# Kernel optimization log

Measured on AMD Instinct MI355X. Metric: run time of the kernel, lower is better.

## Reference

```python
import jax, jax.numpy as jnp
import numpy as np

L = 7
LVL = 3
B = 8
R = 16
N = 4 ** L  # 16384
P = N // 4  # number of local blocks
T = 4 * R   # ConvLocal output features


def build_permutation_indices(L, l):
    delta = 4 ** (L - l - 1)
    tmp = np.tile(np.arange(4) * delta, delta)
    tmp += np.repeat(np.arange(delta), 4)
    tmp = np.tile(tmp, 4 ** l)
    tmp += np.repeat(np.arange(4 ** l) * 4 ** (L - l), 4 ** (L - l))
    return jnp.asarray(tmp, dtype=jnp.int32)


def setup_inputs() -> dict:
    key = jax.random.key(0)
    kx, k1, k2, k3, k4 = jax.random.split(key, 5)
    scale = 1.0 / np.sqrt(T)
    x = jax.random.normal(kx, (B, 2, N, R), dtype=jnp.float32)
    # flax ConvLocal kernels: (out_spatial, kernel_size*in_features, features)
    W_rr = jax.random.normal(k1, (P, 4 * R, T), dtype=jnp.float32) * scale
    W_ri = jax.random.normal(k2, (P, 4 * R, T), dtype=jnp.float32) * scale
    W_ir = jax.random.normal(k3, (P, 4 * R, T), dtype=jnp.float32) * scale
    W_ii = jax.random.normal(k4, (P, 4 * R, T), dtype=jnp.float32) * scale
    perm_idx = build_permutation_indices(L, LVL)
    return {"x": x, "W_rr": W_rr, "W_ri": W_ri, "W_ir": W_ir,
            "W_ii": W_ii, "perm_idx": perm_idx}


def reference(x, W_rr, W_ri, W_ir, W_ii, perm_idx):
    b, _, n, r = x.shape
    p = n // 4
    # butterfly permutation gather along the spatial axis
    xp = jnp.take(x, perm_idx, axis=2)            # [B, 2, n, r]
    # group into length-4 windows; flax ConvLocal flattens (kernel, in_feat)
    xr = xp[:, 0].reshape(b, p, 4 * r)            # [B, p, 4r]
    xi = xp[:, 1].reshape(b, p, 4 * r)
    # block-diagonal (locally connected) matmuls, complex-style combine
    y_re = jnp.einsum('bpi,pio->bpo', xr, W_rr) + jnp.einsum('bpi,pio->bpo', xi, W_ri)
    y_im = jnp.einsum('bpi,pio->bpo', xr, W_ir) + jnp.einsum('bpi,pio->bpo', xi, W_ii)
    y = jnp.stack([y_re, y_im], axis=1)           # [B, 2, p, 4r]
    return y.reshape(b, 2, n, r)
```

## Files before the change

### kernel.cpp

```cpp
#include <hip/hip_runtime.h>

#define C_N 16384
#define C_R 16
#define C_P 4096
#define C_B 8

__global__ __launch_bounds__(256, 8)
void butterfly_local_conv(const float* __restrict__ x,
                          const float* __restrict__ Wrr,
                          const float* __restrict__ Wri,
                          const float* __restrict__ Wir,
                          const float* __restrict__ Wii,
                          const int*   __restrict__ perm,
                          float* __restrict__ out)
{
    __shared__ float xs[2][C_B][64];
    __shared__ float partial[4][2][C_B][64];

    const int t = threadIdx.x;
    const int p = blockIdx.x;

    {
        const int c = t >> 7;
        const int b = (t >> 4) & 7;
        const int s = (t >> 2) & 3;
        const int q = t & 3;
        const int n = perm[4 * p + s];
        const float4 v = ((const float4*)(x + (((size_t)(b * 2 + c)) * C_N + n) * C_R))[q];
        ((float4*)&xs[c][b][0])[s * 4 + q] = v;
    }
    __syncthreads();

    const int w = t >> 6;
    const int o = t & 63;
    const int ibase = w * 16;

    float acc_re[C_B], acc_im[C_B];
    #pragma unroll
    for (int b = 0; b < C_B; ++b) { acc_re[b] = 0.0f; acc_im[b] = 0.0f; }

    const size_t wbase = (size_t)p * 64 * 64 + (size_t)ibase * 64 + o;
    const float* __restrict__ wrr_p = Wrr + wbase;
    const float* __restrict__ wri_p = Wri + wbase;
    const float* __restrict__ wir_p = Wir + wbase;
    const float* __restrict__ wii_p = Wii + wbase;

    #pragma unroll
    for (int k0 = 0; k0 < 16; k0 += 4) {
        float wrr[4], wri[4], wir[4], wii[4];
        #pragma unroll
        for (int k = 0; k < 4; ++k) {
            const int off = (k0 + k) * 64;
            wrr[k] = wrr_p[off];
            wri[k] = wri_p[off];
            wir[k] = wir_p[off];
            wii[k] = wii_p[off];
        }
        #pragma unroll
        for (int b = 0; b < C_B; ++b) {
            const float4 xr4 = *(const float4*)(&xs[0][b][ibase + k0]);
            const float4 xi4 = *(const float4*)(&xs[1][b][ibase + k0]);
            acc_re[b] = fmaf(xr4.x, wrr[0], acc_re[b]);
            acc_re[b] = fmaf(xi4.x, wri[0], acc_re[b]);
            acc_im[b] = fmaf(xr4.x, wir[0], acc_im[b]);
            acc_im[b] = fmaf(xi4.x, wii[0], acc_im[b]);

            acc_re[b] = fmaf(xr4.y, wrr[1], acc_re[b]);
            acc_re[b] = fmaf(xi4.y, wri[1], acc_re[b]);
            acc_im[b] = fmaf(xr4.y, wir[1], acc_im[b]);
            acc_im[b] = fmaf(xi4.y, wii[1], acc_im[b]);

            acc_re[b] = fmaf(xr4.z, wrr[2], acc_re[b]);
            acc_re[b] = fmaf(xi4.z, wri[2], acc_re[b]);
            acc_im[b] = fmaf(xr4.z, wir[2], acc_im[b]);
            acc_im[b] = fmaf(xi4.z, wii[2], acc_im[b]);

            acc_re[b] = fmaf(xr4.w, wrr[3], acc_re[b]);
            acc_re[b] = fmaf(xi4.w, wri[3], acc_re[b]);
            acc_im[b] = fmaf(xr4.w, wir[3], acc_im[b]);
            acc_im[b] = fmaf(xi4.w, wii[3], acc_im[b]);
        }
    }

    #pragma unroll
    for (int b = 0; b < C_B; ++b) {
        partial[w][0][b][o] = acc_re[b];
        partial[w][1][b][o] = acc_im[b];
    }
    __syncthreads();

    #pragma unroll
    for (int j = 0; j < 4; ++j) {
        const int cb = (t >> 6) * 4 + j;
        const int c = cb >> 3;
        const int b = cb & 7;
        const float s = partial[0][c][b][o] + partial[1][c][b][o]
                      + partial[2][c][b][o] + partial[3][c][b][o];
        out[((size_t)(b * 2 + c)) * (C_N * C_R) + (size_t)p * 64 + o] = s;
    }
}

extern "C" void kernel_launch(void* const* d_in, const int* in_sizes, int n_in,
                              void* d_out, int out_size, void* d_ws, size_t ws_size,
                              hipStream_t stream) {
    const float* x    = (const float*)d_in[0];
    const float* Wrr  = (const float*)d_in[1];
    const float* Wri  = (const float*)d_in[2];
    const float* Wir  = (const float*)d_in[3];
    const float* Wii  = (const float*)d_in[4];
    const int*   perm = (const int*)d_in[5];
    float* out = (float*)d_out;

    butterfly_local_conv<<<dim3(C_P), dim3(256), 0, stream>>>(
        x, Wrr, Wri, Wir, Wii, perm, out);
}
```

Baseline: 268.8 us.

## Use single-wavefront blocks with register double-buffered weight prefetch

Each block shrinks from 256 threads to a single 64-lane wavefront. Every lane now computes the full 64-input reduction for one output column, which removes the shared-memory partial-sum buffer, both __syncthreads calls and the cross-wave reduction. Weights are streamed in chunks of eight rows into two register buffers, so the next chunk's loads overlap the FMAs on the current one. The costs are much higher register pressure (64 buffer floats plus accumulators) and less parallelism per block, and the x gather now uses fewer lanes, each loading four float4s. The missing barrier after the xs store is safe only because the block is exactly one wavefront.

```diff
diff --git a/kernel.cpp b/kernel.cpp
--- a/kernel.cpp
+++ b/kernel.cpp
@@ -5,7 +5,7 @@
 #define C_P 4096
 #define C_B 8
 
-__global__ __launch_bounds__(256, 8)
+__global__ __launch_bounds__(64, 4)
 void butterfly_local_conv(const float* __restrict__ x,
                           const float* __restrict__ Wrr,
                           const float* __restrict__ Wri,
@@ -15,88 +15,78 @@
                           float* __restrict__ out)
 {
     __shared__ float xs[2][C_B][64];
-    __shared__ float partial[4][2][C_B][64];
 
-    const int t = threadIdx.x;
-    const int p = blockIdx.x;
+    const int lane = threadIdx.x;
+    const int p    = blockIdx.x;
+
+    const int sc = lane >> 5;
+    const int sb = (lane >> 2) & 7;
+    const int ss = lane & 3;
+    const int n  = perm[4 * p + ss];
+    const float4* xsrc = (const float4*)(x + (((size_t)(sb * 2 + sc)) * C_N + n) * C_R);
+    const float4 v0 = xsrc[0], v1 = xsrc[1], v2 = xsrc[2], v3 = xsrc[3];
+
+    const size_t wbase = (size_t)p * 64 * 64 + lane;
+    const float* __restrict__ prr = Wrr + wbase;
+    const float* __restrict__ pri = Wri + wbase;
+    const float* __restrict__ pir = Wir + wbase;
+    const float* __restrict__ pii = Wii + wbase;
+
+    float buf0[32], buf1[32];
+    #pragma unroll
+    for (int k = 0; k < 8; ++k) {
+        buf0[k]      = prr[k * 64];
+        buf0[8 + k]  = pri[k * 64];
+        buf0[16 + k] = pir[k * 64];
+        buf0[24 + k] = pii[k * 64];
+    }
 
     {
-        const int c = t >> 7;
-        const int b = (t >> 4) & 7;
-        const int s = (t >> 2) & 3;
-        const int q = t & 3;
-        const int n = perm[4 * p + s];
-        const float4 v = ((const float4*)(x + (((size_t)(b * 2 + c)) * C_N + n) * C_R))[q];
-        ((float4*)&xs[c][b][0])[s * 4 + q] = v;
+        float4* dst = (float4*)(&xs[sc][sb][ss * 16]);
+        dst[0] = v0; dst[1] = v1; dst[2] = v2; dst[3] = v3;
     }
-    __syncthreads();
-
-    const int w = t >> 6;
-    const int o = t & 63;
-    const int ibase = w * 16;
 
     float acc_re[C_B], acc_im[C_B];
     #pragma unroll
     for (int b = 0; b < C_B; ++b) { acc_re[b] = 0.0f; acc_im[b] = 0.0f; }
 
-    const size_t wbase = (size_t)p * 64 * 64 + (size_t)ibase * 64 + o;
-    const float* __restrict__ wrr_p = Wrr + wbase;
-    const float* __restrict__ wri_p = Wri + wbase;
-    const float* __restrict__ wir_p = Wir + wbase;
-    const float* __restrict__ wii_p = Wii + wbase;
-
     #pragma unroll
-    for (int k0 = 0; k0 < 16; k0 += 4) {
-        float wrr[4], wri[4], wir[4], wii[4];
-        #pragma unroll
-        for (int k = 0; k < 4; ++k) {
-            const int off = (k0 + k) * 64;
-            wrr[k] = wrr_p[off];
-            wri[k] = wri_p[off];
-            wir[k] = wir_p[off];
-            wii[k] = wii_p[off];
+    for (int ch = 0; ch < 8; ++ch) {
+        float* cur = (ch & 1) ? buf1 : buf0;
+        float* nxt = (ch & 1) ? buf0 : buf1;
+        if (ch < 7) {
+            const int ib = (ch + 1) * 8;
+            #pragma unroll
+            for (int k = 0; k < 8; ++k) {
+                nxt[k]      = prr[(ib + k) * 64];
+                nxt[8 + k]  = pri[(ib + k) * 64];
+                nxt[16 + k] = pir[(ib + k) * 64];
+                nxt[24 + k] = pii[(ib + k) * 64];
+            }
         }
+        const int i0 = ch * 8;
         #pragma unroll
         for (int b = 0; b < C_B; ++b) {
-            const float4 xr4 = *(const float4*)(&xs[0][b][ibase + k0]);
-            const float4 xi4 = *(const float4*)(&xs[1][b][ibase + k0]);
-            acc_re[b] = fmaf(xr4.x, wrr[0], acc_re[b]);
-            acc_re[b] = fmaf(xi4.x, wri[0], acc_re[b]);
-            acc_im[b] = fmaf(xr4.x, wir[0], acc_im[b]);
-            acc_im[b] = fmaf(xi4.x, wii[0], acc_im[b]);
-
-            acc_re[b] = fmaf(xr4.y, wrr[1], acc_re[b]);
-            acc_re[b] = fmaf(xi4.y, wri[1], acc_re[b]);
-            acc_im[b] = fmaf(xr4.y, wir[1], acc_im[b]);
-            acc_im[b] = fmaf(xi4.y, wii[1], acc_im[b]);
-
-            acc_re[b] = fmaf(xr4.z, wrr[2], acc_re[b]);
-            acc_re[b] = fmaf(xi4.z, wri[2], acc_re[b]);
-            acc_im[b] = fmaf(xr4.z, wir[2], acc_im[b]);
-            acc_im[b] = fmaf(xi4.z, wii[2], acc_im[b]);
-
-            acc_re[b] = fmaf(xr4.w, wrr[3], acc_re[b]);
-            acc_re[b] = fmaf(xi4.w, wri[3], acc_re[b]);
-            acc_im[b] = fmaf(xr4.w, wir[3], acc_im[b]);
-            acc_im[b] = fmaf(xi4.w, wii[3], acc_im[b]);
+            float xr[8], xi[8];
+            *(float4*)&xr[0] = *(const float4*)(&xs[0][b][i0]);
+            *(float4*)&xr[4] = *(const float4*)(&xs[0][b][i0 + 4]);
+            *(float4*)&xi[0] = *(const float4*)(&xs[1][b][i0]);
+            *(float4*)&xi[4] = *(const float4*)(&xs[1][b][i0 + 4]);
+            #pragma unroll
+            for (int k = 0; k < 8; ++k) {
+                acc_re[b] = fmaf(xr[k], cur[k],      acc_re[b]);
+                acc_re[b] = fmaf(xi[k], cur[8 + k],  acc_re[b]);
+                acc_im[b] = fmaf(xr[k], cur[16 + k], acc_im[b]);
+                acc_im[b] = fmaf(xi[k], cur[24 + k], acc_im[b]);
+            }
         }
     }
 
+    const size_t obase = (size_t)p * 64 + lane;
     #pragma unroll
     for (int b = 0; b < C_B; ++b) {
-        partial[w][0][b][o] = acc_re[b];
-        partial[w][1][b][o] = acc_im[b];
-    }
-    __syncthreads();
-
-    #pragma unroll
-    for (int j = 0; j < 4; ++j) {
-        const int cb = (t >> 6) * 4 + j;
-        const int c = cb >> 3;
-        const int b = cb & 7;
-        const float s = partial[0][c][b][o] + partial[1][c][b][o]
-                      + partial[2][c][b][o] + partial[3][c][b][o];
-        out[((size_t)(b * 2 + c)) * (C_N * C_R) + (size_t)p * 64 + o] = s;
+        out[((size_t)(b * 2 + 0)) * (C_N * C_R) + obase] = acc_re[b];
+        out[((size_t)(b * 2 + 1)) * (C_N * C_R) + obase] = acc_im[b];
     }
 }
 
@@ -111,6 +101,6 @@
     const int*   perm = (const int*)d_in[5];
     float* out = (float*)d_out;
 
-    butterfly_local_conv<<<dim3(C_P), dim3(256), 0, stream>>>(
+    butterfly_local_conv<<<dim3(C_P), dim3(64), 0, stream>>>(
         x, Wrr, Wri, Wir, Wii, perm, out);
 }
```

Measured after the change: 273.2 us. No clear change (+1.6%).
